# Kernel tuning notes

Measured on AMD Instinct MI355X. Metric: run time of the kernel, lower is better.

Reference implementation:

```python
import jax, jax.numpy as jnp
import numpy as np

B, T, S, H, E = 4, 2048, 2048, 16, 64  # batch, q_len, kv_len, heads, head_dim


def setup_inputs() -> dict:
    key = jax.random.key(0)
    kq, kk, kv, kl, kw = jax.random.split(key, 5)
    query = jax.random.normal(kq, (B, T, H * E), dtype=jnp.float32)
    key_t = jax.random.normal(kk, (B, S, H * E), dtype=jnp.float32)
    value = jax.random.normal(kv, (B, S, H * E), dtype=jnp.float32)
    # valid lengths in [S//2, S] so every row has at least one attendable key
    lengths = jax.random.randint(kl, (B,), S // 2, S + 1)
    key_padding_mask = jnp.arange(S)[None, :] < lengths[:, None]  # (B, S) bool, True = keep
    W_out = jax.random.normal(kw, (H * E, E), dtype=jnp.float32) * 0.02
    b_out = jnp.zeros((E,), dtype=jnp.float32)
    return {"query": query, "key": key_t, "value": value,
            "key_padding_mask": key_padding_mask, "W_out": W_out, "b_out": b_out}


def reference(query, key, value, key_padding_mask, W_out, b_out):
    # (B, N, H*E) -> (B, H, N, E)
    q = query.reshape(B, T, H, E).transpose(0, 2, 1, 3)
    k = key.reshape(B, S, H, E).transpose(0, 2, 1, 3)
    v = value.reshape(B, S, H, E).transpose(0, 2, 1, 3)
    softmax_temp = 1.0 / np.sqrt(E).astype(np.float32)
    scores = jnp.einsum('bhte,bhse->bhts', q * softmax_temp, k)  # (B,H,T,S)
    neg_inf = jnp.finfo(scores.dtype).min
    scores = jnp.where(key_padding_mask[:, None, None, :], scores, neg_inf)
    attn = jax.nn.softmax(scores, axis=-1)  # dropout p=0 -> identity
    out = jnp.einsum('bhts,bhsd->bthd', attn, v)  # (B,T,H,E)
    out = out.reshape(B * T, H * E)
    return out @ W_out + b_out  # (B*T, E)
```

## Files before the change

kernel.cpp:

```cpp
#include <hip/hip_runtime.h>
#include <hip/hip_bf16.h>

#define Bq 4
#define Tq 2048
#define Sq 2048
#define Hq 16
#define Eq 64
#define HEq 1024

typedef __attribute__((ext_vector_type(8))) _Float16 half8;
typedef __attribute__((ext_vector_type(16))) float f32x16;

#define AS1 __attribute__((address_space(1)))
#define AS3 __attribute__((address_space(3)))

__device__ __forceinline__ void gl_lds16(const void* g, void* l) {
  __builtin_amdgcn_global_load_lds((const AS1 unsigned*)g, (AS3 unsigned*)l, 16, 0, 0);
}
#define VMCNT(n) asm volatile("s_waitcnt vmcnt(" #n ")" ::: "memory")
#define LGKM0 asm volatile("s_waitcnt lgkmcnt(0)" ::: "memory")

#if __has_builtin(__builtin_amdgcn_exp2f)
#define EXP2F(x) __builtin_amdgcn_exp2f(x)
#else
#define EXP2F(x) exp2f(x)
#endif

__device__ __forceinline__ unsigned pk16(float a, float b) {
  return __builtin_bit_cast(unsigned, __builtin_amdgcn_cvt_pkrtz(a, b));
}

__global__ __launch_bounds__(256) void prep_kernel(
    const float* __restrict__ K, const float* __restrict__ V,
    const float* __restrict__ W, const void* __restrict__ mask,
    char* __restrict__ KP, char* __restrict__ VP,
    _Float16* __restrict__ WT, int* __restrict__ lens) {
  __shared__ _Float16 tile[64][72];
  const int bid = blockIdx.x;
  const int tid = threadIdx.x;

  if (bid < 4096) {
    const int isV = bid >= 2048;
    const int b2 = bid & 2047;
    const int t = b2 & 31, h = (b2 >> 5) & 15, b = b2 >> 9;
    const int s0 = t * 64;
    const int s_in = tid >> 2, e0 = (tid & 3) * 16;
    const float* X = isV ? V : K;
    const float* src = X + ((size_t)(b * Sq + s0 + s_in) * HEq + h * Eq + e0);
#pragma unroll
    for (int i = 0; i < 4; ++i) {
      const float4 f = *(const float4*)(src + i * 4);
      tile[s_in][e0 + i * 4 + 0] = (_Float16)f.x;
      tile[s_in][e0 + i * 4 + 1] = (_Float16)f.y;
      tile[s_in][e0 + i * 4 + 2] = (_Float16)f.z;
      tile[s_in][e0 + i * 4 + 3] = (_Float16)f.w;
    }
    __syncthreads();
    half8 u0, u1;
    if (!isV) {
      const int gi = tid >> 5, sl = (tid & 31) * 2;
#pragma unroll
      for (int j = 0; j < 8; ++j) {
        u0[j] = tile[sl][gi * 8 + j];
        u1[j] = tile[sl + 1][gi * 8 + j];
      }
      char* dst = KP + ((size_t)b2 * 8192) + tid * 32;
      *(half8*)dst = u0;
      *(half8*)(dst + 16) = u1;
    } else {
      const int sgi = tid >> 5, e = (tid & 31) * 2;
#pragma unroll
      for (int j = 0; j < 8; ++j) {
        u0[j] = tile[sgi * 8 + j][e];
        u1[j] = tile[sgi * 8 + j][e + 1];
      }
      char* dst = VP + ((size_t)b2 * 8192) + tid * 32;
      *(half8*)dst = u0;
      *(half8*)(dst + 16) = u1;
    }
  } else if (bid < 4352) {
    const int id = (bid - 4096) * 256 + tid;
    const int n = id >> 10, k = id & 1023;
    WT[id] = (_Float16)W[k * Eq + n];
  } else if (tid < 64) {
    const int b = bid - 4352;
    const int lane = tid;
    const unsigned w0 = *(const unsigned*)mask;
    int cnt = 0;
    if (w0 == 1u) {
      const int* m = (const int*)mask + b * Sq;
      for (int s = lane; s < Sq; s += 64) cnt += (m[s] != 0);
    } else if (w0 == 0x3F800000u) {
      const float* m = (const float*)mask + b * Sq;
      for (int s = lane; s < Sq; s += 64) cnt += (m[s] != 0.f);
    } else {
      const unsigned char* m = (const unsigned char*)mask + b * Sq;
      for (int s = lane; s < Sq; s += 64) cnt += (m[s] != 0);
    }
    for (int o = 32; o; o >>= 1) cnt += __shfl_down(cnt, o);
    if (lane == 0) lens[b] = cnt;
  }
}

__global__ __launch_bounds__(512, 4) void flash_kernel(
    const float* __restrict__ Q, const char* __restrict__ KP,
    const char* __restrict__ VP, const int* __restrict__ lens,
    _Float16* __restrict__ attnO) {
  __shared__ __align__(16) _Float16 KV[2][2][4096];

  const int bid = blockIdx.x;
  const int qt = bid >> 6;
  const int h = (bid >> 2) & 15;
  const int b = ((bid & 3) + (bid >> 8)) & 3;
  const int tid = threadIdx.x;
  const int w = tid >> 6, lane = tid & 63;
  const int qq = lane & 31, hi = lane >> 5;
  const int len = lens[b];
  const int q0 = qt * 256 + w * 32;

  const float qscale = 0.125f * 1.44269504088896340736f;
  half8 qf[4];
  {
    const float* qrow = Q + ((size_t)(b * Tq + q0 + qq) * HEq + h * Eq);
#pragma unroll
    for (int kw = 0; kw < 4; ++kw) {
      const float4 f0 = *(const float4*)(qrow + kw * 16 + hi * 8);
      const float4 f1 = *(const float4*)(qrow + kw * 16 + hi * 8 + 4);
      half8 qv;
      qv[0] = (_Float16)(f0.x * qscale);
      qv[1] = (_Float16)(f0.y * qscale);
      qv[2] = (_Float16)(f0.z * qscale);
      qv[3] = (_Float16)(f0.w * qscale);
      qv[4] = (_Float16)(f1.x * qscale);
      qv[5] = (_Float16)(f1.y * qscale);
      qv[6] = (_Float16)(f1.z * qscale);
      qv[7] = (_Float16)(f1.w * qscale);
      qf[kw] = qv;
    }
  }

  f32x16 Oa[2];
#pragma unroll
  for (int i = 0; i < 2; ++i)
#pragma unroll
    for (int r = 0; r < 16; ++r) Oa[i][r] = 0.f;
  float ls0 = 0.f, ls1 = 0.f;

  const char* kpb = KP + (size_t)(b * Hq + h) * 32 * 8192;
  const char* vpb = VP + (size_t)(b * Hq + h) * 32 * 8192;
  const int so = w * 1024 + lane * 16;

  const int ntiles = (len + 63) >> 6;

  gl_lds16(kpb + so, (char*)&KV[0][0][0] + so);
  gl_lds16(vpb + so, (char*)&KV[0][1][0] + so);

  int p = 0;
  for (int t = 0; t < ntiles; ++t) {
    if (t + 1 < ntiles) {
      const size_t tb = (size_t)(t + 1) * 8192;
      gl_lds16(kpb + tb + so, (char*)&KV[p ^ 1][0][0] + so);
      gl_lds16(vpb + tb + so, (char*)&KV[p ^ 1][1][0] + so);
      VMCNT(2);
    } else {
      VMCNT(0);
    }
    __builtin_amdgcn_s_barrier();
    __builtin_amdgcn_sched_barrier(0);

    __builtin_amdgcn_s_setprio(1);
    f32x16 sc[2];
#pragma unroll
    for (int sm = 0; sm < 2; ++sm) {
      f32x16 acc;
#pragma unroll
      for (int r = 0; r < 16; ++r) acc[r] = 0.f;
#pragma unroll
      for (int kw = 0; kw < 4; ++kw) {
        const half8 kf = *(const half8*)((const char*)&KV[p][0][0] +
                                         (kw * 2 + hi) * 1024 + (sm * 32 + qq) * 16);
        acc = __builtin_amdgcn_mfma_f32_32x32x16_f16(kf, qf[kw], acc, 0, 0, 0);
      }
      sc[sm] = acc;
    }
    __builtin_amdgcn_s_setprio(0);

    const int svalid = len - (t << 6);
    if (svalid < 64) {
#pragma unroll
      for (int r = 0; r < 16; ++r) {
        const int sl = (r & 3) + 8 * (r >> 2) + 4 * hi;
        if (sl >= svalid) sc[0][r] = -60000.f;
        if (32 + sl >= svalid) sc[1][r] = -60000.f;
      }
    }

    unsigned pku[2][4][2];
#pragma unroll
    for (int sm = 0; sm < 2; ++sm)
#pragma unroll
      for (int rb = 0; rb < 4; ++rb)
#pragma unroll
        for (int pp = 0; pp < 2; ++pp) {
          const float a0 = EXP2F(sc[sm][rb * 4 + pp * 2]);
          const float a1 = EXP2F(sc[sm][rb * 4 + pp * 2 + 1]);
          ls0 += a0;
          ls1 += a1;
          pku[sm][rb][pp] = pk16(a0, a1);
        }

#pragma unroll
    for (int kw = 0; kw < 4; ++kw) {
      const int sm = kw >> 1;
      const int rbe = (kw & 1) * 2, rbo = rbe + 1;
      union { unsigned u[4]; half8 h; } pu;
#pragma unroll
      for (int pp = 0; pp < 2; ++pp) {
        const unsigned ev = pku[sm][rbe][pp];
        const unsigned od = pku[sm][rbo][pp];
        const unsigned sendv = hi ? ev : od;
        const unsigned recvv = __shfl_xor(sendv, 32);
        pu.u[pp] = hi ? recvv : ev;
        pu.u[2 + pp] = hi ? od : recvv;
      }
      const half8 pf = pu.h;
      __builtin_amdgcn_s_setprio(1);
#pragma unroll
      for (int eh = 0; eh < 2; ++eh) {
        const half8 vf = *(const half8*)((const char*)&KV[p][1][0] +
                                         (kw * 2 + hi) * 1024 + (eh * 32 + qq) * 16);
        Oa[eh] = __builtin_amdgcn_mfma_f32_32x32x16_f16(vf, pf, Oa[eh], 0, 0, 0);
      }
      __builtin_amdgcn_s_setprio(0);
    }

    __builtin_amdgcn_s_barrier();
    __builtin_amdgcn_sched_barrier(0);
    p ^= 1;
  }

  float ls = ls0 + ls1;
  ls += __shfl_xor(ls, 32);
  const float inv = 1.f / ls;
  char* const scratch = (char*)&KV[0][0][0] + w * 4096;
#pragma unroll
  for (int eh = 0; eh < 2; ++eh)
#pragma unroll
    for (int rb = 0; rb < 4; ++rb)
#pragma unroll
      for (int pp = 0; pp < 2; ++pp) {
        const int e0 = eh * 32 + rb * 8 + hi * 4 + pp * 2;
        const unsigned uo = pk16(Oa[eh][rb * 4 + pp * 2] * inv,
                                 Oa[eh][rb * 4 + pp * 2 + 1] * inv);
        *(unsigned*)(scratch + qq * 128 + ((e0 * 2) ^ ((qq & 7) << 4))) = uo;
      }
  LGKM0;
  __builtin_amdgcn_sched_barrier(0);
#pragma unroll
  for (int i = 0; i < 4; ++i) {
    const int qr = i * 8 + (lane >> 3), ch = lane & 7;
    const half8 ov = *(const half8*)(scratch + qr * 128 + ((ch * 16) ^ ((qr & 7) << 4)));
    *(half8*)(attnO + (size_t)(b * Tq + q0 + qr) * HEq + h * Eq + ch * 8) = ov;
  }
}

typedef __attribute__((ext_vector_type(4))) float floatx4;
__global__ __launch_bounds__(256) void proj_kernel(
    const _Float16* __restrict__ A, const _Float16* __restrict__ WT,
    const float* __restrict__ bias, float* __restrict__ out) {
  const int tid = threadIdx.x;
  const int w = tid >> 6, lane = tid & 63;
  const int g = lane >> 4, c = lane & 15;
  const int r0 = blockIdx.x * 64 + w * 16;
  floatx4 acc[4];
#pragma unroll
  for (int i = 0; i < 4; ++i) acc[i] = (floatx4){0.f, 0.f, 0.f, 0.f};
  const _Float16* arow = A + (size_t)(r0 + c) * HEq;
  for (int kc = 0; kc < 32; ++kc) {
    const half8 af = *(const half8*)(arow + kc * 32 + g * 8);
#pragma unroll
    for (int nt = 0; nt < 4; ++nt) {
      const half8 bf =
          *(const half8*)(WT + (size_t)(nt * 16 + c) * HEq + kc * 32 + g * 8);
      acc[nt] = __builtin_amdgcn_mfma_f32_16x16x32_f16(af, bf, acc[nt], 0, 0, 0);
    }
  }
#pragma unroll
  for (int r = 0; r < 4; ++r) {
    const int row = r0 + g * 4 + r;
#pragma unroll
    for (int nt = 0; nt < 4; ++nt) {
      const int col = nt * 16 + c;
      out[(size_t)row * Eq + col] = acc[nt][r] + bias[col];
    }
  }
}

extern "C" void kernel_launch(void* const* d_in, const int* in_sizes, int n_in,
                              void* d_out, int out_size, void* d_ws, size_t ws_size,
                              hipStream_t stream) {
  const float* q = (const float*)d_in[0];
  const float* k = (const float*)d_in[1];
  const float* v = (const float*)d_in[2];
  const void* mask = d_in[3];
  const float* W = (const float*)d_in[4];
  const float* bias = (const float*)d_in[5];
  float* out = (float*)d_out;

  char* ws = (char*)d_ws;
  int* lens = (int*)ws;
  _Float16* WT = (_Float16*)(ws + 256);
  _Float16* attn = (_Float16*)(ws + (256 + 131072));
  char* KP = ws + (256 + 131072 + (1 << 24));
  char* VP = ws + (256 + 131072 + (1 << 24) + (1 << 24));

  prep_kernel<<<4356, 256, 0, stream>>>(k, v, W, mask, KP, VP, WT, lens);
  flash_kernel<<<512, 512, 0, stream>>>(q, KP, VP, lens, attn);
  proj_kernel<<<(Bq * Tq) / 64, 256, 0, stream>>>(attn, WT, bias, out);
}
```

Before: 108.4 us.

## Deepen flash K/V prefetch to a four-buffer ring and split projection blocks

The attention kernel's K/V staging moves from a double buffer to a four-slot LDS ring that prefetches two tiles ahead. That lets it drop the trailing per-iteration barrier and wait with vmcnt(4) instead of vmcnt(2). Tail prefetches are clamped to the last tile so the wait counts stay uniform. The cost is twice the LDS per block, which could limit co-residency. Separately, the projection kernel now launches twice as many 128-thread blocks of 32 rows each, to spread that GEMM over more CUs.

```diff
diff --git a/kernel.cpp b/kernel.cpp
--- a/kernel.cpp
+++ b/kernel.cpp
@@ -106,7 +106,7 @@
     const float* __restrict__ Q, const char* __restrict__ KP,
     const char* __restrict__ VP, const int* __restrict__ lens,
     _Float16* __restrict__ attnO) {
-  __shared__ __align__(16) _Float16 KV[2][2][4096];
+  __shared__ __align__(16) _Float16 KV[4][2][4096];
 
   const int bid = blockIdx.x;
   const int qt = bid >> 6;
@@ -150,24 +150,29 @@
   const char* vpb = VP + (size_t)(b * Hq + h) * 32 * 8192;
   const int so = w * 1024 + lane * 16;
 
-  const int ntiles = (len + 63) >> 6;
+  const int nt = (len + 63) >> 6;
 
   gl_lds16(kpb + so, (char*)&KV[0][0][0] + so);
   gl_lds16(vpb + so, (char*)&KV[0][1][0] + so);
-
-  int p = 0;
-  for (int t = 0; t < ntiles; ++t) {
-    if (t + 1 < ntiles) {
-      const size_t tb = (size_t)(t + 1) * 8192;
-      gl_lds16(kpb + tb + so, (char*)&KV[p ^ 1][0][0] + so);
-      gl_lds16(vpb + tb + so, (char*)&KV[p ^ 1][1][0] + so);
-      VMCNT(2);
-    } else {
-      VMCNT(0);
-    }
+  gl_lds16(kpb + 8192 + so, (char*)&KV[1][0][0] + so);
+  gl_lds16(vpb + 8192 + so, (char*)&KV[1][1][0] + so);
+
+  for (int t = 0; t < nt; ++t) {
+    {
+      const int tp = (t + 2 < nt) ? t + 2 : nt - 1;
+      const size_t tb = (size_t)tp * 8192;
+      char* kd = (char*)&KV[(t + 2) & 3][0][0] + so;
+      char* vd = (char*)&KV[(t + 2) & 3][1][0] + so;
+      gl_lds16(kpb + tb + so, kd);
+      gl_lds16(vpb + tb + so, vd);
+    }
+    VMCNT(4);
     __builtin_amdgcn_s_barrier();
     __builtin_amdgcn_sched_barrier(0);
 
+    const char* kbuf = (const char*)&KV[t & 3][0][0];
+    const char* vbuf = (const char*)&KV[t & 3][1][0];
+
     __builtin_amdgcn_s_setprio(1);
     f32x16 sc[2];
 #pragma unroll
@@ -177,8 +182,8 @@
       for (int r = 0; r < 16; ++r) acc[r] = 0.f;
 #pragma unroll
       for (int kw = 0; kw < 4; ++kw) {
-        const half8 kf = *(const half8*)((const char*)&KV[p][0][0] +
-                                         (kw * 2 + hi) * 1024 + (sm * 32 + qq) * 16);
+        const half8 kf = *(const half8*)(kbuf + (kw * 2 + hi) * 1024 +
+                                         (sm * 32 + qq) * 16);
         acc = __builtin_amdgcn_mfma_f32_32x32x16_f16(kf, qf[kw], acc, 0, 0, 0);
       }
       sc[sm] = acc;
@@ -227,17 +232,17 @@
       __builtin_amdgcn_s_setprio(1);
 #pragma unroll
       for (int eh = 0; eh < 2; ++eh) {
-        const half8 vf = *(const half8*)((const char*)&KV[p][1][0] +
-                                         (kw * 2 + hi) * 1024 + (eh * 32 + qq) * 16);
+        const half8 vf = *(const half8*)(vbuf + (kw * 2 + hi) * 1024 +
+                                         (eh * 32 + qq) * 16);
         Oa[eh] = __builtin_amdgcn_mfma_f32_32x32x16_f16(vf, pf, Oa[eh], 0, 0, 0);
       }
       __builtin_amdgcn_s_setprio(0);
     }
-
-    __builtin_amdgcn_s_barrier();
-    __builtin_amdgcn_sched_barrier(0);
-    p ^= 1;
-  }
+  }
+
+  VMCNT(0);
+  __builtin_amdgcn_s_barrier();
+  __builtin_amdgcn_sched_barrier(0);
 
   float ls = ls0 + ls1;
   ls += __shfl_xor(ls, 32);
@@ -248,10 +253,10 @@
 #pragma unroll
     for (int rb = 0; rb < 4; ++rb)
 #pragma unroll
-      for (int pp = 0; pp < 2; ++pp) {
-        const int e0 = eh * 32 + rb * 8 + hi * 4 + pp * 2;
-        const unsigned uo = pk16(Oa[eh][rb * 4 + pp * 2] * inv,
-                                 Oa[eh][rb * 4 + pp * 2 + 1] * inv);
+      for (int pp2 = 0; pp2 < 2; ++pp2) {
+        const int e0 = eh * 32 + rb * 8 + hi * 4 + pp2 * 2;
+        const unsigned uo = pk16(Oa[eh][rb * 4 + pp2 * 2] * inv,
+                                 Oa[eh][rb * 4 + pp2 * 2 + 1] * inv);
         *(unsigned*)(scratch + qq * 128 + ((e0 * 2) ^ ((qq & 7) << 4))) = uo;
       }
   LGKM0;
@@ -265,13 +270,13 @@
 }
 
 typedef __attribute__((ext_vector_type(4))) float floatx4;
-__global__ __launch_bounds__(256) void proj_kernel(
+__global__ __launch_bounds__(128) void proj_kernel(
     const _Float16* __restrict__ A, const _Float16* __restrict__ WT,
     const float* __restrict__ bias, float* __restrict__ out) {
   const int tid = threadIdx.x;
   const int w = tid >> 6, lane = tid & 63;
   const int g = lane >> 4, c = lane & 15;
-  const int r0 = blockIdx.x * 64 + w * 16;
+  const int r0 = blockIdx.x * 32 + w * 16;
   floatx4 acc[4];
 #pragma unroll
   for (int i = 0; i < 4; ++i) acc[i] = (floatx4){0.f, 0.f, 0.f, 0.f};
@@ -312,9 +317,9 @@
   _Float16* WT = (_Float16*)(ws + 256);
   _Float16* attn = (_Float16*)(ws + (256 + 131072));
   char* KP = ws + (256 + 131072 + (1 << 24));
-  char* VP = ws + (256 + 131072 + (1 << 24) + (1 << 24));
+  char* VP = ws + (256 + 131072 + 2 * (1 << 24));
 
   prep_kernel<<<4356, 256, 0, stream>>>(k, v, W, mask, KP, VP, WT, lens);
   flash_kernel<<<512, 512, 0, stream>>>(q, KP, VP, lens, attn);
-  proj_kernel<<<(Bq * Tq) / 64, 256, 0, stream>>>(attn, WT, bias, out);
-}
+  proj_kernel<<<256, 128, 0, stream>>>(attn, WT, bias, out);
+}
```

New measurement: 101.0 us. -6.8%, faster.
